# Kernel tuning notes

Hardware: AMD Instinct MI355X
Metric: run time of the kernel (lower is better)

The kernel has to match this reference:

```python
import jax, jax.numpy as jnp
import numpy as np

DIM = 768
EPS = 1e-06


def _layernorm(x, gamma, beta):
    # LayerNorm over last axis (channels), eps=EPS, elementwise affine
    mu = jnp.mean(x, axis=-1, keepdims=True)
    var = jnp.mean(jnp.square(x - mu), axis=-1, keepdims=True)
    return (x - mu) * jax.lax.rsqrt(var + EPS) * gamma + beta


def setup_inputs() -> dict:
    key = jax.random.key(0)
    ks = jax.random.split(key, 10)
    B, C, H, W = 16, DIM, 32, 32
    s = 1.0 / np.sqrt(C)  # mimic Conv2d default init scale
    return {
        "x": jax.random.normal(ks[0], (B, C, H, W), dtype=jnp.float32),
        "W1": jax.random.uniform(ks[1], (C, C), jnp.float32, -s, s),
        "b1": jax.random.uniform(ks[2], (C,), jnp.float32, -s, s),
        "g1": jnp.ones((C,), jnp.float32),
        "beta1": jnp.zeros((C,), jnp.float32),
        "W2": jax.random.uniform(ks[3], (C, C), jnp.float32, -s, s),
        "b2": jax.random.uniform(ks[4], (C,), jnp.float32, -s, s),
        "g2": jnp.ones((C,), jnp.float32),
        "beta2": jnp.zeros((C,), jnp.float32),
        "W3": jax.random.uniform(ks[5], (C, C), jnp.float32, -s, s),
        "b3": jax.random.uniform(ks[6], (C,), jnp.float32, -s, s),
    }


def reference(x, W1, b1, g1, beta1, W2, b2, g2, beta2, W3, b3):
    # x: [B, C, H, W] (NCHW). Work in NHWC; 1x1 conv == channel matmul.
    h = jnp.transpose(x, (0, 2, 3, 1))  # [B, H, W, C]
    h = jnp.einsum("bhwc,oc->bhwo", h, W1) + b1
    h = jax.nn.gelu(_layernorm(h, g1, beta1), approximate=False)
    h = jnp.einsum("bhwc,oc->bhwo", h, W2) + b2
    h = jax.nn.gelu(_layernorm(h, g2, beta2), approximate=False)
    h = jnp.einsum("bhwc,oc->bhwo", h, W3) + b3
    return jnp.transpose(h, (0, 3, 1, 2))  # back to NCHW
```

## Files before the change

### kernel.cpp

```cpp
#include <hip/hip_runtime.h>
#include <hip/hip_bf16.h>

typedef __bf16 bf16;
typedef __bf16 bf16x4 __attribute__((ext_vector_type(4)));
typedef __bf16 bf16x8 __attribute__((ext_vector_type(8)));
typedef float f32x4 __attribute__((ext_vector_type(4)));

#define DIM 768
#define HW 1024
#define BATCH 16
#define M_TOTAL (BATCH * HW)
#define NKT 24

#define AS1 __attribute__((address_space(1)))
#define AS3 __attribute__((address_space(3)))


__global__ void prep_kernel(const float* __restrict__ x, bf16* __restrict__ xb,
                            const float4* __restrict__ w1, const float4* __restrict__ w2,
                            const float4* __restrict__ w3,
                            bf16x8* __restrict__ o1, bf16x8* __restrict__ o2,
                            bf16x8* __restrict__ o3) {
    __shared__ float tile[32][33];
    if (blockIdx.x < 864) {
        const int b = blockIdx.x;
        const int which = b / 288;
        const int i = (b % 288) * 256 + threadIdx.x;
        const float4* w = which == 0 ? w1 : which == 1 ? w2 : w3;
        bf16x8* o = which == 0 ? o1 : which == 1 ? o2 : o3;
        const int row = i / 96, br = i % 96;
        const int q = br >> 2, g = br & 3;
        float4 lo = w[row * 192 + q * 8 + g];
        float4 hi = w[row * 192 + q * 8 + g + 4];
        bf16x8 r = { (bf16)lo.x, (bf16)lo.y, (bf16)lo.z, (bf16)lo.w,
                     (bf16)hi.x, (bf16)hi.y, (bf16)hi.z, (bf16)hi.w };
        o[row * 96 + br] = r;
    } else {
        const int e = blockIdx.x - 864;
        const int b = e / 768;
        const int rem = e % 768;
        const int c0 = (rem / 32) * 32;
        const int hw0 = (rem % 32) * 32;
        const int tx = threadIdx.x & 31, ty = threadIdx.x >> 5;

        const float* src = x + ((size_t)b * DIM + c0) * HW + hw0;
#pragma unroll
        for (int j = 0; j < 4; j++)
            tile[ty + 8 * j][tx] = src[(size_t)(ty + 8 * j) * HW + tx];
        __syncthreads();
        const int ptx = (((tx & 15) >> 2) << 3) + (tx & 3) + ((tx >> 4) << 2);
        bf16* dst = xb + ((size_t)b * HW + hw0) * DIM + c0;
#pragma unroll
        for (int j = 0; j < 4; j++)
            dst[(size_t)(ty + 8 * j) * DIM + ptx] = (bf16)tile[tx][ty + 8 * j];
    }
}

template <int MODE>
__global__ __launch_bounds__(256, 4) void gemm_kernel(
    const bf16* __restrict__ A,
    const bf16* __restrict__ Bw,
    const float* __restrict__ bias,
    void* __restrict__ out)
{
    constexpr int K = DIM;
    __shared__ bf16 S[2][256][32];

    const int t = threadIdx.x;
    const int lane = t & 63;
    const int w = t >> 6;

    const int bid = blockIdx.x;
    const int virt = (bid & 7) * 128 + (bid >> 3);
    const int m0 = (virt >> 2) * 64;
    const int n0 = (virt & 3) * 192;

    const int fr = lane & 15, fq = lane >> 4;

    f32x4 acc[4][3] = {};

    const int sg = t & 3;

    auto stage = [&](int kt, int buf) {
        const int k0 = kt * 32;
#pragma unroll
        for (int j = 0; j < 4; j++) {
            const int r = j * 64 + (t >> 2);
            const int gs = sg ^ ((r ^ (r >> 2)) & 3);
            const bf16* src = (j == 0)
                ? (A  + (size_t)(m0 + r) * K + k0 + gs * 8)
                : (Bw + (size_t)(n0 + r - 64) * K + k0 + gs * 8);
            __builtin_amdgcn_global_load_lds((const AS1 void*)src,
                (AS3 void*)&S[buf][r][sg * 8], 16, 0, 0);
        }
    };

    stage(0, 0);
    asm volatile("s_waitcnt vmcnt(0)" ::: "memory");
    __builtin_amdgcn_s_barrier();
    __builtin_amdgcn_sched_barrier(0);

    int cur = 0;
    for (int kt = 0; kt < NKT; ++kt) {
        bf16x8 aF[4], bF[3];
#pragma unroll
        for (int mi = 0; mi < 4; mi++) {
            const int R = mi * 16 + fr;
            aF[mi] = *(const bf16x8*)(&S[cur][R][0] + ((fq ^ ((R ^ (R >> 2)) & 3)) << 3));
        }
#pragma unroll
        for (int ni = 0; ni < 3; ni++) {
            const int R = 64 + w * 48 + ni * 16 + fr;
            bF[ni] = *(const bf16x8*)(&S[cur][R][0] + ((fq ^ ((R ^ (R >> 2)) & 3)) << 3));
        }
        if (kt + 1 < NKT) stage(kt + 1, cur ^ 1);

        __builtin_amdgcn_s_setprio(1);
#pragma unroll
        for (int mi = 0; mi < 4; mi++)
#pragma unroll
            for (int ni = 0; ni < 3; ni++)
                acc[mi][ni] = __builtin_amdgcn_mfma_f32_16x16x32_bf16(aF[mi], bF[ni], acc[mi][ni], 0, 0, 0);
        __builtin_amdgcn_s_setprio(0);

        if (kt + 1 < NKT) {
            asm volatile("s_waitcnt vmcnt(0)" ::: "memory");
            __builtin_amdgcn_s_barrier();
            __builtin_amdgcn_sched_barrier(0);
        }
        cur ^= 1;
    }

    if (MODE == 0) {
        bf16* o = (bf16*)out;
#pragma unroll
        for (int mi = 0; mi < 4; mi++) {
            const int row = m0 + mi * 16 + fq * 4;
#pragma unroll
            for (int ni = 0; ni < 3; ni++) {
                const int off = w * 48 + ni * 16;
                const int col = n0 + off + fr;
                const int pcol = n0 + (off & ~31) + ((fr >> 2) << 3) + (fr & 3)
                               + (((off >> 4) & 1) << 2);
                const float bv = bias[col];
#pragma unroll
                for (int r = 0; r < 4; r++)
                    o[(size_t)(row + r) * DIM + pcol] = (bf16)(acc[mi][ni][r] + bv);
            }
        }
    } else {
        float* o = (float*)out;
#pragma unroll
        for (int mi = 0; mi < 4; mi++) {
            const int nb = m0 + mi * 16 + fq * 4;
            const int bI = nb >> 10, hw = nb & 1023;
#pragma unroll
            for (int ni = 0; ni < 3; ni++) {
                const int col = n0 + w * 48 + ni * 16 + fr;
                f32x4 v = acc[mi][ni] + bias[col];
                *(f32x4*)(o + ((size_t)bI * DIM + col) * HW + hw) = v;
            }
        }
    }
}

__global__ __launch_bounds__(256) void ln_gelu_kernel(
    bf16* __restrict__ h, const float* __restrict__ g, const float* __restrict__ beta)
{
    const int wave = threadIdx.x >> 6;
    const int lane = threadIdx.x & 63;
    const int n = blockIdx.x * 4 + wave;
    bf16* row = h + (size_t)n * DIM;

    float v[12];
    float s = 0.f, ss = 0.f;
#pragma unroll
    for (int j = 0; j < 3; j++) {
        bf16x4 x = *(const bf16x4*)(row + j * 256 + lane * 4);
#pragma unroll
        for (int i = 0; i < 4; i++) {
            float f = (float)x[i];
            v[j * 4 + i] = f;
            s += f;
            ss += f * f;
        }
    }
#pragma unroll
    for (int off = 32; off > 0; off >>= 1) {
        s += __shfl_xor(s, off);
        ss += __shfl_xor(ss, off);
    }
    const float mu = s * (1.f / DIM);
    const float var = ss * (1.f / DIM) - mu * mu;
    const float rstd = rsqrtf(var + 1e-6f);

#pragma unroll
    for (int j = 0; j < 3; j++) {
        bf16x4 r;
#pragma unroll
        for (int i = 0; i < 4; i++) {
            const int c = j * 256 + lane * 4 + i;
            const int p = (lane * 4 + i) & 31;
            const int kk = ((p >> 3) << 2) + (p & 7) + ((p & 4) ? 12 : 0);
            const int gi = (c & ~31) + kk;
            float y = (v[j * 4 + i] - mu) * rstd * g[gi] + beta[gi];
            y = 0.5f * y * (1.f + erff(y * 0.70710678118f));
            r[i] = (bf16)y;
        }
        *(bf16x4*)(row + j * 256 + lane * 4) = r;
    }
}

extern "C" void kernel_launch(void* const* d_in, const int* in_sizes, int n_in,
                              void* d_out, int out_size, void* d_ws, size_t ws_size,
                              hipStream_t stream) {
    const float* x   = (const float*)d_in[0];
    const float* W1  = (const float*)d_in[1];
    const float* b1  = (const float*)d_in[2];
    const float* g1  = (const float*)d_in[3];
    const float* be1 = (const float*)d_in[4];
    const float* W2  = (const float*)d_in[5];
    const float* b2  = (const float*)d_in[6];
    const float* g2  = (const float*)d_in[7];
    const float* be2 = (const float*)d_in[8];
    const float* W3  = (const float*)d_in[9];
    const float* b3  = (const float*)d_in[10];
    float* out = (float*)d_out;

    bf16* Wb1  = (bf16*)d_ws;
    bf16* Wb2  = Wb1 + (size_t)DIM * DIM;
    bf16* Wb3  = Wb2 + (size_t)DIM * DIM;
    bf16* buf0 = Wb3 + (size_t)DIM * DIM;
    bf16* buf1 = buf0 + (size_t)M_TOTAL * DIM;

    prep_kernel<<<864 + 12288, 256, 0, stream>>>(
        x, buf0, (const float4*)W1, (const float4*)W2, (const float4*)W3,
        (bf16x8*)Wb1, (bf16x8*)Wb2, (bf16x8*)Wb3);

    const int ggrid = (M_TOTAL / 64) * (DIM / 192);
    gemm_kernel<0><<<ggrid, 256, 0, stream>>>(buf0, Wb1, b1, buf1);
    ln_gelu_kernel<<<M_TOTAL / 4, 256, 0, stream>>>(buf1, g1, be1);
    gemm_kernel<0><<<ggrid, 256, 0, stream>>>(buf1, Wb2, b2, buf0);
    ln_gelu_kernel<<<M_TOTAL / 4, 256, 0, stream>>>(buf0, g2, be2);
    gemm_kernel<1><<<ggrid, 256, 0, stream>>>(buf0, Wb3, b3, out);
}
```

Baseline: 169.8 us.

## Replace LDS-staged GEMM with direct global-to-register fragment loads

The GEMM no longer stages A and B tiles through shared memory with global_load_lds and barriers. Each wave now loads its MFMA fragments straight from global memory into registers, with two register sets used as a ping-pong prefetch. The warp layout also changes from 4 waves splitting N to a 2x2 wave grid of 32x96 per wave. This removes LDS traffic and block-wide barriers, but each wave re-reads data that other waves also load, which leans on L1/L2 and raises register pressure.

```diff
diff --git a/kernel.cpp b/kernel.cpp
--- a/kernel.cpp
+++ b/kernel.cpp
@@ -11,9 +11,6 @@
 #define BATCH 16
 #define M_TOTAL (BATCH * HW)
 #define NKT 24
-
-#define AS1 __attribute__((address_space(1)))
-#define AS3 __attribute__((address_space(3)))
 
 
 __global__ void prep_kernel(const float* __restrict__ x, bf16* __restrict__ xb,
@@ -63,12 +60,10 @@
     const float* __restrict__ bias,
     void* __restrict__ out)
 {
-    constexpr int K = DIM;
-    __shared__ bf16 S[2][256][32];
-
     const int t = threadIdx.x;
     const int lane = t & 63;
-    const int w = t >> 6;
+    const int wave = t >> 6;
+    const int wm = wave >> 1, wn = wave & 1;
 
     const int bid = blockIdx.x;
     const int virt = (bid & 7) * 128 + (bid >> 3);
@@ -77,68 +72,59 @@
 
     const int fr = lane & 15, fq = lane >> 4;
 
-    f32x4 acc[4][3] = {};
-
-    const int sg = t & 3;
-
-    auto stage = [&](int kt, int buf) {
-        const int k0 = kt * 32;
-#pragma unroll
-        for (int j = 0; j < 4; j++) {
-            const int r = j * 64 + (t >> 2);
-            const int gs = sg ^ ((r ^ (r >> 2)) & 3);
-            const bf16* src = (j == 0)
-                ? (A  + (size_t)(m0 + r) * K + k0 + gs * 8)
-                : (Bw + (size_t)(n0 + r - 64) * K + k0 + gs * 8);
-            __builtin_amdgcn_global_load_lds((const AS1 void*)src,
-                (AS3 void*)&S[buf][r][sg * 8], 16, 0, 0);
-        }
-    };
-
-    stage(0, 0);
-    asm volatile("s_waitcnt vmcnt(0)" ::: "memory");
-    __builtin_amdgcn_s_barrier();
-    __builtin_amdgcn_sched_barrier(0);
-
-    int cur = 0;
-    for (int kt = 0; kt < NKT; ++kt) {
-        bf16x8 aF[4], bF[3];
-#pragma unroll
-        for (int mi = 0; mi < 4; mi++) {
-            const int R = mi * 16 + fr;
-            aF[mi] = *(const bf16x8*)(&S[cur][R][0] + ((fq ^ ((R ^ (R >> 2)) & 3)) << 3));
-        }
-#pragma unroll
-        for (int ni = 0; ni < 3; ni++) {
-            const int R = 64 + w * 48 + ni * 16 + fr;
-            bF[ni] = *(const bf16x8*)(&S[cur][R][0] + ((fq ^ ((R ^ (R >> 2)) & 3)) << 3));
-        }
-        if (kt + 1 < NKT) stage(kt + 1, cur ^ 1);
-
-        __builtin_amdgcn_s_setprio(1);
-#pragma unroll
-        for (int mi = 0; mi < 4; mi++)
-#pragma unroll
-            for (int ni = 0; ni < 3; ni++)
-                acc[mi][ni] = __builtin_amdgcn_mfma_f32_16x16x32_bf16(aF[mi], bF[ni], acc[mi][ni], 0, 0, 0);
-        __builtin_amdgcn_s_setprio(0);
-
-        if (kt + 1 < NKT) {
-            asm volatile("s_waitcnt vmcnt(0)" ::: "memory");
-            __builtin_amdgcn_s_barrier();
-            __builtin_amdgcn_sched_barrier(0);
-        }
-        cur ^= 1;
-    }
+    int aOff[2], bOff[6];
+#pragma unroll
+    for (int mi = 0; mi < 2; mi++)
+        aOff[mi] = (m0 + wm * 32 + mi * 16 + fr) * DIM + fq * 8;
+#pragma unroll
+    for (int ni = 0; ni < 6; ni++)
+        bOff[ni] = (n0 + wn * 96 + ni * 16 + fr) * DIM + fq * 8;
+
+    f32x4 acc[2][6] = {};
+    bf16x8 aP[2], bP[6], aQ[2], bQ[6];
+
+#define LD_P(kt) do { \
+    _Pragma("unroll") for (int mi = 0; mi < 2; mi++) \
+        aP[mi] = *(const bf16x8*)(A + aOff[mi] + (kt) * 32); \
+    _Pragma("unroll") for (int ni = 0; ni < 6; ni++) \
+        bP[ni] = *(const bf16x8*)(Bw + bOff[ni] + (kt) * 32); } while (0)
+#define LD_Q(kt) do { \
+    _Pragma("unroll") for (int mi = 0; mi < 2; mi++) \
+        aQ[mi] = *(const bf16x8*)(A + aOff[mi] + (kt) * 32); \
+    _Pragma("unroll") for (int ni = 0; ni < 6; ni++) \
+        bQ[ni] = *(const bf16x8*)(Bw + bOff[ni] + (kt) * 32); } while (0)
+#define MM_P() do { __builtin_amdgcn_s_setprio(1); \
+    _Pragma("unroll") for (int mi = 0; mi < 2; mi++) \
+    _Pragma("unroll") for (int ni = 0; ni < 6; ni++) \
+        acc[mi][ni] = __builtin_amdgcn_mfma_f32_16x16x32_bf16(aP[mi], bP[ni], acc[mi][ni], 0, 0, 0); \
+    __builtin_amdgcn_s_setprio(0); } while (0)
+#define MM_Q() do { __builtin_amdgcn_s_setprio(1); \
+    _Pragma("unroll") for (int mi = 0; mi < 2; mi++) \
+    _Pragma("unroll") for (int ni = 0; ni < 6; ni++) \
+        acc[mi][ni] = __builtin_amdgcn_mfma_f32_16x16x32_bf16(aQ[mi], bQ[ni], acc[mi][ni], 0, 0, 0); \
+    __builtin_amdgcn_s_setprio(0); } while (0)
+
+    LD_P(0);
+#pragma unroll 2
+    for (int kt = 0; kt < NKT; kt += 2) {
+        LD_Q(kt + 1);
+        MM_P();
+        if (kt + 2 < NKT) LD_P(kt + 2);
+        MM_Q();
+    }
+#undef LD_P
+#undef LD_Q
+#undef MM_P
+#undef MM_Q
 
     if (MODE == 0) {
         bf16* o = (bf16*)out;
 #pragma unroll
-        for (int mi = 0; mi < 4; mi++) {
-            const int row = m0 + mi * 16 + fq * 4;
-#pragma unroll
-            for (int ni = 0; ni < 3; ni++) {
-                const int off = w * 48 + ni * 16;
+        for (int mi = 0; mi < 2; mi++) {
+            const int row = m0 + wm * 32 + mi * 16 + fq * 4;
+#pragma unroll
+            for (int ni = 0; ni < 6; ni++) {
+                const int off = wn * 96 + ni * 16;
                 const int col = n0 + off + fr;
                 const int pcol = n0 + (off & ~31) + ((fr >> 2) << 3) + (fr & 3)
                                + (((off >> 4) & 1) << 2);
@@ -151,12 +137,12 @@
     } else {
         float* o = (float*)out;
 #pragma unroll
-        for (int mi = 0; mi < 4; mi++) {
-            const int nb = m0 + mi * 16 + fq * 4;
+        for (int mi = 0; mi < 2; mi++) {
+            const int nb = m0 + wm * 32 + mi * 16 + fq * 4;
             const int bI = nb >> 10, hw = nb & 1023;
 #pragma unroll
-            for (int ni = 0; ni < 3; ni++) {
-                const int col = n0 + w * 48 + ni * 16 + fr;
+            for (int ni = 0; ni < 6; ni++) {
+                const int col = n0 + wn * 96 + ni * 16 + fr;
                 f32x4 v = acc[mi][ni] + bias[col];
                 *(f32x4*)(o + ((size_t)bI * DIM + col) * HW + hw) = v;
             }
```

New measurement: 427.6 us. 152% more time.
